# Optimization experiments

Hardware: AMD Instinct MI355X
Metric: run time of the kernel (lower is better)

Reference implementation:

```python
import jax, jax.numpy as jnp
import numpy as np

NUM_NODES = 50000
NUM_EDGES = 800000
DIM = 128


def setup_inputs() -> dict:
    key = jax.random.key(0)
    k0, k1, k2, k3 = jax.random.split(key, 4)
    edge_index = jax.random.randint(k0, (2, NUM_EDGES), 0, NUM_NODES, dtype=jnp.int64)
    emb = jax.random.normal(k1, (NUM_NODES, DIM), dtype=jnp.float32) * 0.02
    s = 1.0 / np.sqrt(DIM)
    W1 = jax.random.normal(k2, (DIM, DIM), dtype=jnp.float32) * s
    b1 = jnp.zeros((DIM,), dtype=jnp.float32)
    W2 = jax.random.normal(k3, (DIM, DIM), dtype=jnp.float32) * s
    b2 = jnp.zeros((DIM,), dtype=jnp.float32)
    return {"edge_index": edge_index, "emb": emb, "W1": W1, "b1": b1, "W2": W2, "b2": b2}


def gcn_conv(x, W, b, src, dst, num_nodes):
    # PyG GCNConv: h = x @ W; out = D^{-1/2}(A+I)D^{-1/2} h + b
    h = x @ W  # [N, D]
    deg = jnp.zeros((num_nodes,), h.dtype).at[dst].add(1.0) + 1.0  # +1 self-loop
    dis = jax.lax.rsqrt(deg)  # deg >= 1 always
    msg = h[src] * (dis[src] * dis[dst])[:, None]  # [E, D]
    agg = jax.ops.segment_sum(msg, dst, num_segments=num_nodes)
    agg = agg + h * (dis * dis)[:, None]  # self-loop term: norm = 1/deg
    return agg + b


def reference(edge_index, emb, W1, b1, W2, b2):
    src, dst = edge_index[0], edge_index[1]
    x = gcn_conv(emb, W1, b1, src, dst, NUM_NODES)
    x = jax.nn.relu(x)
    x = gcn_conv(x, W2, b2, src, dst, NUM_NODES)
    return x
```

## Files before the change

kernel.cpp:

```cpp
#include <hip/hip_runtime.h>
#include <hip/hip_fp16.h>

#define DIM 128
#define SEG 64
#define CAP 60

typedef _Float16 half8 __attribute__((ext_vector_type(8)));
typedef float floatx4 __attribute__((ext_vector_type(4)));


__global__ __launch_bounds__(256) void k_init_pack(unsigned short* __restrict__ csr, int N,
                                                   const float* __restrict__ W1,
                                                   const float* __restrict__ W2,
                                                   _Float16* __restrict__ Wp) {
    int i = blockIdx.x * 256 + threadIdx.x;
    int gs = gridDim.x * 256;
    if (i < 32768) {
        int sel = i >> 14;
        int flat = i & 16383;
        int f = flat >> 9;
        int rest = flat & 511;
        int lane = rest >> 3, j = rest & 7;
        int t = f >> 2, s = f & 3;
        int k = s * 32 + (lane >> 4) * 8 + j;
        int n = t * 16 + (lane & 15);
        const float* W = sel ? W2 : W1;
        Wp[(size_t)sel * 16384 + flat] = (_Float16)W[k * DIM + n];
    }
    const uint4 ff = make_uint4(~0u, ~0u, ~0u, ~0u);
    const uint4 head = make_uint4(0u, 0u, ~0u, ~0u);
    int total = N * 8;
    for (int j2 = i; j2 < total; j2 += gs)
        ((uint4*)csr)[j2] = ((j2 & 7) == 0) ? head : ff;
}


__global__ __launch_bounds__(256) void k_fill(const int* __restrict__ ei,
                                              unsigned short* __restrict__ csr,
                                              int E, int N) {
    int e = blockIdx.x * 256 + threadIdx.x;
    if (e < E) {
        int sv = ei[e];
        int dv = ei[E + e];
        if ((unsigned)sv < (unsigned)N && (unsigned)dv < (unsigned)N) {
            int pos = atomicAdd((int*)(csr + (size_t)dv * SEG), 1);
            if (pos < CAP) csr[(size_t)dv * SEG + 4 + pos] = (unsigned short)sv;
        }
    }
}


__global__ __launch_bounds__(256) void k_gemm1(const float* __restrict__ X,
                                               const unsigned short* __restrict__ csr,
                                               const _Float16* __restrict__ Wp,
                                               __half* __restrict__ out, int N) {
    __shared__ _Float16 ls[64 * 136];
    int tid = threadIdx.x;
    int w = tid >> 6, lane = tid & 63;
    int m = lane & 15, q = lane >> 4;
    int row0 = blockIdx.x * 64 + w * 16;

    int arow = row0 + m;
    bool okA = arow < N;
    half8 a[4];
#pragma unroll
    for (int s = 0; s < 4; ++s) {
        if (okA) {
            const float* Xa = X + (size_t)arow * DIM + s * 32 + q * 8;
            float4 f0 = *(const float4*)Xa;
            float4 f1 = *(const float4*)(Xa + 4);
            half8 h;
            h[0] = (_Float16)f0.x; h[1] = (_Float16)f0.y;
            h[2] = (_Float16)f0.z; h[3] = (_Float16)f0.w;
            h[4] = (_Float16)f1.x; h[5] = (_Float16)f1.y;
            h[6] = (_Float16)f1.z; h[7] = (_Float16)f1.w;
            a[s] = h;
        } else {
            a[s] = (half8)(_Float16)0.0f;
        }
    }
    int drow = row0 + q * 4;
    float dd[4];
#pragma unroll
    for (int r = 0; r < 4; ++r) {
        int rr2 = drow + r;
        int c = (rr2 < N) ? *(const int*)(csr + (size_t)rr2 * SEG) : 0;
        dd[r] = rsqrtf((float)c + 1.0f);
    }

    _Float16* lrow = ls + w * 16 * 136;
#pragma unroll
    for (int t = 0; t < 8; ++t) {
        floatx4 acc = {0.f, 0.f, 0.f, 0.f};
#pragma unroll
        for (int s = 0; s < 4; ++s) {
            half8 b = *(const half8*)(Wp + ((size_t)(t * 4 + s) * 64 + lane) * 8);
            acc = __builtin_amdgcn_mfma_f32_16x16x32_f16(a[s], b, acc, 0, 0, 0);
        }
#pragma unroll
        for (int r = 0; r < 4; ++r)
            lrow[(q * 4 + r) * 136 + t * 16 + m] = (_Float16)(acc[r] * dd[r]);
    }
    __syncthreads();

    int rr = lane >> 2, cc = (lane & 3) * 32;
    int grow = row0 + rr;
    if (grow < N) {
        const uint4* lsrc = (const uint4*)(lrow + rr * 136 + cc);
        uint4* gdst = (uint4*)((__half*)out + (size_t)grow * DIM + cc);
        gdst[0] = lsrc[0];
        gdst[1] = lsrc[1];
        gdst[2] = lsrc[2];
        gdst[3] = lsrc[3];
    }
}


__global__ __launch_bounds__(256) void k_aggemm(const __half* __restrict__ hn,
                                                const unsigned short* __restrict__ csr,
                                                const float* __restrict__ bias,
                                                const _Float16* __restrict__ Wp2,
                                                __half* __restrict__ hn2, int N) {
    __shared__ __align__(16) _Float16 As[16 * 136];
    __shared__ __align__(16) _Float16 Os[16 * 136];
    __shared__ float sdis[16];
    int tid = threadIdx.x;
    int slot = tid >> 4;
    int node = blockIdx.x * 16 + slot;
    int c8 = (tid & 15) << 3;

    float4 bv0 = *(const float4*)(bias + c8);
    float4 bv1 = *(const float4*)(bias + c8 + 4);
    float bb[8] = {bv0.x, bv0.y, bv0.z, bv0.w, bv1.x, bv1.y, bv1.z, bv1.w};
    const uint4 z4 = make_uint4(0u, 0u, 0u, 0u);
    const ushort4 sent = make_ushort4(0xFFFFu, 0xFFFFu, 0xFFFFu, 0xFFFFu);

    union { __half2 h[4]; uint4 u; } pu;
    pu.u = make_uint4(0u, 0u, 0u, 0u);
    float sc = 0.f;
    if (node < N) {
        const unsigned short* seg = csr + (size_t)node * SEG;
        int cnt = *(const int*)seg;
        uint4 selfv = *(const uint4*)(hn + (size_t)node * DIM + c8);
        sc = rsqrtf((float)cnt + 1.0f);
        int pcnt = (cnt + 3) & ~3;
        if (pcnt > CAP) pcnt = CAP;
        const unsigned short* slots = seg + 4;

        float acc[8];
#pragma unroll
        for (int j = 0; j < 8; ++j) acc[j] = 0.f;

        ushort4 ss = (pcnt > 0) ? *(const ushort4*)slots : sent;
        for (int e0 = 0; e0 < pcnt; e0 += 4) {
            ushort4 ssn = (e0 + 4 < pcnt) ? *(const ushort4*)(slots + e0 + 4) : sent;
            uint4 v0 = (ss.x != 0xFFFFu) ? *(const uint4*)(hn + (size_t)ss.x * DIM + c8) : z4;
            uint4 v1 = (ss.y != 0xFFFFu) ? *(const uint4*)(hn + (size_t)ss.y * DIM + c8) : z4;
            uint4 v2 = (ss.z != 0xFFFFu) ? *(const uint4*)(hn + (size_t)ss.z * DIM + c8) : z4;
            uint4 v3 = (ss.w != 0xFFFFu) ? *(const uint4*)(hn + (size_t)ss.w * DIM + c8) : z4;
            const __half2* h0 = (const __half2*)&v0;
            const __half2* h1 = (const __half2*)&v1;
            const __half2* h2 = (const __half2*)&v2;
            const __half2* h3 = (const __half2*)&v3;
#pragma unroll
            for (int j = 0; j < 4; ++j) {
                float2 f0 = __half22float2(h0[j]);
                float2 f1 = __half22float2(h1[j]);
                float2 f2 = __half22float2(h2[j]);
                float2 f3 = __half22float2(h3[j]);
                acc[2 * j]     += (f0.x + f1.x) + (f2.x + f3.x);
                acc[2 * j + 1] += (f0.y + f1.y) + (f2.y + f3.y);
            }
            ss = ssn;
        }

        const __half2* hs = (const __half2*)&selfv;
        float o[8];
#pragma unroll
        for (int j = 0; j < 4; ++j) {
            float2 fs = __half22float2(hs[j]);
            o[2 * j]     = (acc[2 * j]     + fs.x) * sc + bb[2 * j];
            o[2 * j + 1] = (acc[2 * j + 1] + fs.y) * sc + bb[2 * j + 1];
        }
        pu.h[0] = __floats2half2_rn(fmaxf(o[0], 0.f), fmaxf(o[1], 0.f));
        pu.h[1] = __floats2half2_rn(fmaxf(o[2], 0.f), fmaxf(o[3], 0.f));
        pu.h[2] = __floats2half2_rn(fmaxf(o[4], 0.f), fmaxf(o[5], 0.f));
        pu.h[3] = __floats2half2_rn(fmaxf(o[6], 0.f), fmaxf(o[7], 0.f));
    }
    *(uint4*)((char*)As + slot * 272 + (tid & 15) * 16) = pu.u;
    if ((tid & 15) == 0) sdis[slot] = sc;
    __syncthreads();

    int w = tid >> 6, lane = tid & 63;
    int m = lane & 15, q = lane >> 4;
    half8 a[4];
#pragma unroll
    for (int s = 0; s < 4; ++s)
        a[s] = *(const half8*)((const char*)As + m * 272 + s * 64 + q * 16);
    float dd[4];
#pragma unroll
    for (int r = 0; r < 4; ++r) dd[r] = sdis[q * 4 + r];

#pragma unroll
    for (int ti = 0; ti < 2; ++ti) {
        int t = w * 2 + ti;
        floatx4 acc2 = {0.f, 0.f, 0.f, 0.f};
#pragma unroll
        for (int s = 0; s < 4; ++s) {
            half8 b = *(const half8*)(Wp2 + ((size_t)(t * 4 + s) * 64 + lane) * 8);
            acc2 = __builtin_amdgcn_mfma_f32_16x16x32_f16(a[s], b, acc2, 0, 0, 0);
        }
#pragma unroll
        for (int r = 0; r < 4; ++r)
            Os[(q * 4 + r) * 136 + t * 16 + m] = (_Float16)(acc2[r] * dd[r]);
    }
    __syncthreads();

    int rr3 = tid >> 4, ci = tid & 15;
    int grow = blockIdx.x * 16 + rr3;
    if (grow < N)
        *(uint4*)((__half*)hn2 + (size_t)grow * DIM + ci * 8) =
            *(const uint4*)((const char*)Os + rr3 * 272 + ci * 16);
}


__global__ __launch_bounds__(256) void k_agg_out(const __half* __restrict__ hn,
                                                 const unsigned short* __restrict__ csr,
                                                 const float* __restrict__ bias,
                                                 float* __restrict__ outf, int N) {
    int tid = threadIdx.x;
    int node = (blockIdx.x * 256 + tid) >> 4;
    int c8 = (tid & 15) << 3;
    if (node >= N) return;

    float4 bv0 = *(const float4*)(bias + c8);
    float4 bv1 = *(const float4*)(bias + c8 + 4);
    float bb[8] = {bv0.x, bv0.y, bv0.z, bv0.w, bv1.x, bv1.y, bv1.z, bv1.w};
    const uint4 z4 = make_uint4(0u, 0u, 0u, 0u);
    const ushort4 sent = make_ushort4(0xFFFFu, 0xFFFFu, 0xFFFFu, 0xFFFFu);

    const unsigned short* seg = csr + (size_t)node * SEG;
    int cnt = *(const int*)seg;
    uint4 selfv = *(const uint4*)(hn + (size_t)node * DIM + c8);
    float sc = rsqrtf((float)cnt + 1.0f);
    int pcnt = (cnt + 3) & ~3;
    if (pcnt > CAP) pcnt = CAP;
    const unsigned short* slots = seg + 4;

    float acc[8];
#pragma unroll
    for (int j = 0; j < 8; ++j) acc[j] = 0.f;

    ushort4 ss = (pcnt > 0) ? *(const ushort4*)slots : sent;
    for (int e0 = 0; e0 < pcnt; e0 += 4) {
        ushort4 ssn = (e0 + 4 < pcnt) ? *(const ushort4*)(slots + e0 + 4) : sent;
        uint4 v0 = (ss.x != 0xFFFFu) ? *(const uint4*)(hn + (size_t)ss.x * DIM + c8) : z4;
        uint4 v1 = (ss.y != 0xFFFFu) ? *(const uint4*)(hn + (size_t)ss.y * DIM + c8) : z4;
        uint4 v2 = (ss.z != 0xFFFFu) ? *(const uint4*)(hn + (size_t)ss.z * DIM + c8) : z4;
        uint4 v3 = (ss.w != 0xFFFFu) ? *(const uint4*)(hn + (size_t)ss.w * DIM + c8) : z4;
        const __half2* h0 = (const __half2*)&v0;
        const __half2* h1 = (const __half2*)&v1;
        const __half2* h2 = (const __half2*)&v2;
        const __half2* h3 = (const __half2*)&v3;
#pragma unroll
        for (int j = 0; j < 4; ++j) {
            float2 f0 = __half22float2(h0[j]);
            float2 f1 = __half22float2(h1[j]);
            float2 f2 = __half22float2(h2[j]);
            float2 f3 = __half22float2(h3[j]);
            acc[2 * j]     += (f0.x + f1.x) + (f2.x + f3.x);
            acc[2 * j + 1] += (f0.y + f1.y) + (f2.y + f3.y);
        }
        ss = ssn;
    }

    const __half2* hs = (const __half2*)&selfv;
    float o[8];
#pragma unroll
    for (int j = 0; j < 4; ++j) {
        float2 fs = __half22float2(hs[j]);
        o[2 * j]     = (acc[2 * j]     + fs.x) * sc + bb[2 * j];
        o[2 * j + 1] = (acc[2 * j + 1] + fs.y) * sc + bb[2 * j + 1];
    }
    *(float4*)(outf + (size_t)node * DIM + c8) = make_float4(o[0], o[1], o[2], o[3]);
    *(float4*)(outf + (size_t)node * DIM + c8 + 4) = make_float4(o[4], o[5], o[6], o[7]);
}


extern "C" void kernel_launch(void* const* d_in, const int* in_sizes, int n_in,
                              void* d_out, int out_size, void* d_ws, size_t ws_size,
                              hipStream_t stream) {
    const int* ei = (const int*)d_in[0];
    const float* emb = (const float*)d_in[1];
    const float* W1 = (const float*)d_in[2];
    const float* b1 = (const float*)d_in[3];
    const float* W2 = (const float*)d_in[4];
    const float* b2 = (const float*)d_in[5];
    float* out = (float*)d_out;

    int E = in_sizes[0] / 2;
    int N = in_sizes[1] / DIM;

    char* p = (char*)d_ws;
    auto alloc = [&](size_t bytes) -> char* {
        char* r = p;
        p += (bytes + 255) & ~(size_t)255;
        return r;
    };
    unsigned short* csr = (unsigned short*)alloc((size_t)N * SEG * 2);
    __half* hn1         = (__half*)alloc((size_t)N * DIM * 2);
    __half* hn2         = (__half*)alloc((size_t)N * DIM * 2);
    _Float16* Wp        = (_Float16*)alloc(2 * 16384 * 2);

    const int GB = (N + 63) / 64;
    const int AB = (N + 15) / 16;

    k_init_pack<<<1024, 256, 0, stream>>>(csr, N, W1, W2, Wp);
    k_fill<<<(E + 255) / 256, 256, 0, stream>>>(ei, csr, E, N);
    k_gemm1<<<GB, 256, 0, stream>>>(emb, csr, Wp, hn1, N);
    k_aggemm<<<AB, 256, 0, stream>>>(hn1, csr, b1, Wp + 16384, hn2, N);
    k_agg_out<<<AB, 256, 0, stream>>>(hn2, csr, b2, out, N);
}
```

Before: 263.9 us.

## Fuse all GCN stages into one persistent cooperative kernel with grid syncs

Replaces the five separate kernel launches with a single cooperative persistent kernel. It runs CSR init, edge fill, first GEMM, fused aggregate+GEMM and final aggregation in sequence, separated by grid.sync barriers. This is meant to remove launch gaps and inter-kernel drain/fill overhead. In exchange the grid is capped at occupancy*CUs (up to 2048 blocks), so per-phase parallelism is limited and grid barriers add cost. The old multi-kernel path is kept as a fallback if the cooperative launch fails.

```diff
diff --git a/kernel.cpp b/kernel.cpp
--- a/kernel.cpp
+++ b/kernel.cpp
@@ -1,5 +1,8 @@
 #include <hip/hip_runtime.h>
 #include <hip/hip_fp16.h>
+#include <hip/hip_cooperative_groups.h>
+
+namespace cg = cooperative_groups;
 
 #define DIM 128
 #define SEG 64
@@ -9,17 +12,284 @@
 typedef float floatx4 __attribute__((ext_vector_type(4)));
 
 
-__global__ __launch_bounds__(256) void k_init_pack(unsigned short* __restrict__ csr, int N,
+__global__ __launch_bounds__(256, 4) void k_gcn(
+    const int* __restrict__ ei, const float* __restrict__ emb,
+    const float* __restrict__ W1, const float* __restrict__ b1,
+    const float* __restrict__ W2, const float* __restrict__ b2,
+    unsigned short* __restrict__ csr, __half* __restrict__ hn1,
+    __half* __restrict__ hn2, _Float16* __restrict__ Wp,
+    float* __restrict__ out, int E, int N)
+{
+    __shared__ __align__(16) char smem[64 * 136 * 2];
+    cg::grid_group grid = cg::this_grid();
+    const int tid = threadIdx.x;
+    const int nb = gridDim.x;
+    const int gtid = blockIdx.x * 256 + tid;
+    const int gs = nb * 256;
+
+    if (gtid < 32768) {
+        int sel = gtid >> 14, flat = gtid & 16383;
+        int f = flat >> 9, rest = flat & 511;
+        int lane = rest >> 3, j = rest & 7;
+        int t = f >> 2, s = f & 3;
+        int k = s * 32 + (lane >> 4) * 8 + j;
+        int n = t * 16 + (lane & 15);
+        const float* W = sel ? W2 : W1;
+        Wp[(size_t)sel * 16384 + flat] = (_Float16)W[k * DIM + n];
+    }
+    {
+        const uint4 ff = make_uint4(~0u, ~0u, ~0u, ~0u);
+        const uint4 head = make_uint4(0u, 0u, ~0u, ~0u);
+        int total = N * 8;
+        for (int j2 = gtid; j2 < total; j2 += gs)
+            ((uint4*)csr)[j2] = ((j2 & 7) == 0) ? head : ff;
+    }
+    __threadfence();
+    grid.sync();
+
+    for (int e = gtid; e < E; e += gs) {
+        int sv = ei[e];
+        int dv = ei[E + e];
+        if ((unsigned)sv < (unsigned)N && (unsigned)dv < (unsigned)N) {
+            int pos = atomicAdd((int*)(csr + (size_t)dv * SEG), 1);
+            if (pos < CAP) csr[(size_t)dv * SEG + 4 + pos] = (unsigned short)sv;
+        }
+    }
+    __threadfence();
+    grid.sync();
+
+    {
+        _Float16* ls = (_Float16*)smem;
+        int w = tid >> 6, lane = tid & 63;
+        int m = lane & 15, q = lane >> 4;
+        int nt = (N + 63) >> 6;
+        for (int tile = blockIdx.x; tile < nt; tile += nb) {
+            int row0 = tile * 64 + w * 16;
+            int arow = row0 + m;
+            bool okA = arow < N;
+            half8 a[4];
+#pragma unroll
+            for (int s = 0; s < 4; ++s) {
+                if (okA) {
+                    const float* Xa = emb + (size_t)arow * DIM + s * 32 + q * 8;
+                    float4 f0 = *(const float4*)Xa;
+                    float4 f1 = *(const float4*)(Xa + 4);
+                    half8 h;
+                    h[0] = (_Float16)f0.x; h[1] = (_Float16)f0.y;
+                    h[2] = (_Float16)f0.z; h[3] = (_Float16)f0.w;
+                    h[4] = (_Float16)f1.x; h[5] = (_Float16)f1.y;
+                    h[6] = (_Float16)f1.z; h[7] = (_Float16)f1.w;
+                    a[s] = h;
+                } else {
+                    a[s] = (half8)(_Float16)0.0f;
+                }
+            }
+            int drow = row0 + q * 4;
+            float dd[4];
+#pragma unroll
+            for (int r = 0; r < 4; ++r) {
+                int rr2 = drow + r;
+                int c = (rr2 < N) ? *(const int*)(csr + (size_t)rr2 * SEG) : 0;
+                dd[r] = rsqrtf((float)c + 1.0f);
+            }
+            _Float16* lrow = ls + w * 16 * 136;
+#pragma unroll
+            for (int t = 0; t < 8; ++t) {
+                floatx4 acc = {0.f, 0.f, 0.f, 0.f};
+#pragma unroll
+                for (int s = 0; s < 4; ++s) {
+                    half8 b = *(const half8*)(Wp + ((size_t)(t * 4 + s) * 64 + lane) * 8);
+                    acc = __builtin_amdgcn_mfma_f32_16x16x32_f16(a[s], b, acc, 0, 0, 0);
+                }
+#pragma unroll
+                for (int r = 0; r < 4; ++r)
+                    lrow[(q * 4 + r) * 136 + t * 16 + m] = (_Float16)(acc[r] * dd[r]);
+            }
+            __syncthreads();
+            int rr = lane >> 2, cc = (lane & 3) * 32;
+            int grow = row0 + rr;
+            if (grow < N) {
+                const uint4* lsrc = (const uint4*)(lrow + rr * 136 + cc);
+                uint4* gdst = (uint4*)((__half*)hn1 + (size_t)grow * DIM + cc);
+                gdst[0] = lsrc[0];
+                gdst[1] = lsrc[1];
+                gdst[2] = lsrc[2];
+                gdst[3] = lsrc[3];
+            }
+            __syncthreads();
+        }
+    }
+    __threadfence();
+    grid.sync();
+
+    {
+        _Float16* As = (_Float16*)smem;
+        _Float16* Os = (_Float16*)(smem + 4352);
+        float* sdis = (float*)(smem + 8704);
+        int slot = tid >> 4;
+        int c8 = (tid & 15) << 3;
+        int w = tid >> 6, lane = tid & 63;
+        int m = lane & 15, q = lane >> 4;
+        float4 bv0 = *(const float4*)(b1 + c8);
+        float4 bv1 = *(const float4*)(b1 + c8 + 4);
+        float bb[8] = {bv0.x, bv0.y, bv0.z, bv0.w, bv1.x, bv1.y, bv1.z, bv1.w};
+        const uint4 z4 = make_uint4(0u, 0u, 0u, 0u);
+        const ushort4 sent = make_ushort4(0xFFFFu, 0xFFFFu, 0xFFFFu, 0xFFFFu);
+        int nt = (N + 15) >> 4;
+        for (int tile = blockIdx.x; tile < nt; tile += nb) {
+            int node = tile * 16 + slot;
+            union { __half2 h[4]; uint4 u; } pu;
+            pu.u = make_uint4(0u, 0u, 0u, 0u);
+            float sc = 0.f;
+            if (node < N) {
+                const unsigned short* seg = csr + (size_t)node * SEG;
+                int cnt = *(const int*)seg;
+                uint4 selfv = *(const uint4*)(hn1 + (size_t)node * DIM + c8);
+                sc = rsqrtf((float)cnt + 1.0f);
+                int pcnt = (cnt + 3) & ~3;
+                if (pcnt > CAP) pcnt = CAP;
+                const unsigned short* slots = seg + 4;
+                float acc[8];
+#pragma unroll
+                for (int j = 0; j < 8; ++j) acc[j] = 0.f;
+                ushort4 ss = (pcnt > 0) ? *(const ushort4*)slots : sent;
+                for (int e0 = 0; e0 < pcnt; e0 += 4) {
+                    ushort4 ssn = (e0 + 4 < pcnt) ? *(const ushort4*)(slots + e0 + 4) : sent;
+                    uint4 v0 = (ss.x != 0xFFFFu) ? *(const uint4*)(hn1 + (size_t)ss.x * DIM + c8) : z4;
+                    uint4 v1 = (ss.y != 0xFFFFu) ? *(const uint4*)(hn1 + (size_t)ss.y * DIM + c8) : z4;
+                    uint4 v2 = (ss.z != 0xFFFFu) ? *(const uint4*)(hn1 + (size_t)ss.z * DIM + c8) : z4;
+                    uint4 v3 = (ss.w != 0xFFFFu) ? *(const uint4*)(hn1 + (size_t)ss.w * DIM + c8) : z4;
+                    const __half2* h0 = (const __half2*)&v0;
+                    const __half2* h1 = (const __half2*)&v1;
+                    const __half2* h2 = (const __half2*)&v2;
+                    const __half2* h3 = (const __half2*)&v3;
+#pragma unroll
+                    for (int j = 0; j < 4; ++j) {
+                        float2 f0 = __half22float2(h0[j]);
+                        float2 f1 = __half22float2(h1[j]);
+                        float2 f2 = __half22float2(h2[j]);
+                        float2 f3 = __half22float2(h3[j]);
+                        acc[2 * j]     += (f0.x + f1.x) + (f2.x + f3.x);
+                        acc[2 * j + 1] += (f0.y + f1.y) + (f2.y + f3.y);
+                    }
+                    ss = ssn;
+                }
+                const __half2* hs = (const __half2*)&selfv;
+                float o[8];
+#pragma unroll
+                for (int j = 0; j < 4; ++j) {
+                    float2 fs = __half22float2(hs[j]);
+                    o[2 * j]     = (acc[2 * j]     + fs.x) * sc + bb[2 * j];
+                    o[2 * j + 1] = (acc[2 * j + 1] + fs.y) * sc + bb[2 * j + 1];
+                }
+                pu.h[0] = __floats2half2_rn(fmaxf(o[0], 0.f), fmaxf(o[1], 0.f));
+                pu.h[1] = __floats2half2_rn(fmaxf(o[2], 0.f), fmaxf(o[3], 0.f));
+                pu.h[2] = __floats2half2_rn(fmaxf(o[4], 0.f), fmaxf(o[5], 0.f));
+                pu.h[3] = __floats2half2_rn(fmaxf(o[6], 0.f), fmaxf(o[7], 0.f));
+            }
+            *(uint4*)((char*)As + slot * 272 + (tid & 15) * 16) = pu.u;
+            if ((tid & 15) == 0) sdis[slot] = sc;
+            __syncthreads();
+
+            half8 a[4];
+#pragma unroll
+            for (int s = 0; s < 4; ++s)
+                a[s] = *(const half8*)((const char*)As + m * 272 + s * 64 + q * 16);
+            float dd[4];
+#pragma unroll
+            for (int r = 0; r < 4; ++r) dd[r] = sdis[q * 4 + r];
+#pragma unroll
+            for (int ti = 0; ti < 2; ++ti) {
+                int t = w * 2 + ti;
+                floatx4 acc2 = {0.f, 0.f, 0.f, 0.f};
+#pragma unroll
+                for (int s = 0; s < 4; ++s) {
+                    half8 b = *(const half8*)(Wp + 16384 + ((size_t)(t * 4 + s) * 64 + lane) * 8);
+                    acc2 = __builtin_amdgcn_mfma_f32_16x16x32_f16(a[s], b, acc2, 0, 0, 0);
+                }
+#pragma unroll
+                for (int r = 0; r < 4; ++r)
+                    Os[(q * 4 + r) * 136 + t * 16 + m] = (_Float16)(acc2[r] * dd[r]);
+            }
+            __syncthreads();
+
+            int rr3 = tid >> 4, ci = tid & 15;
+            int grow = tile * 16 + rr3;
+            if (grow < N)
+                *(uint4*)((__half*)hn2 + (size_t)grow * DIM + ci * 8) =
+                    *(const uint4*)((const char*)Os + rr3 * 272 + ci * 16);
+            __syncthreads();
+        }
+    }
+    __threadfence();
+    grid.sync();
+
+    {
+        int slot0 = gtid >> 4;
+        int c8 = (tid & 15) << 3;
+        int nslots = nb * 16;
+        float4 bv0 = *(const float4*)(b2 + c8);
+        float4 bv1 = *(const float4*)(b2 + c8 + 4);
+        float bb[8] = {bv0.x, bv0.y, bv0.z, bv0.w, bv1.x, bv1.y, bv1.z, bv1.w};
+        const uint4 z4 = make_uint4(0u, 0u, 0u, 0u);
+        const ushort4 sent = make_ushort4(0xFFFFu, 0xFFFFu, 0xFFFFu, 0xFFFFu);
+        for (int node = slot0; node < N; node += nslots) {
+            const unsigned short* seg = csr + (size_t)node * SEG;
+            int cnt = *(const int*)seg;
+            uint4 selfv = *(const uint4*)(hn2 + (size_t)node * DIM + c8);
+            float sc = rsqrtf((float)cnt + 1.0f);
+            int pcnt = (cnt + 3) & ~3;
+            if (pcnt > CAP) pcnt = CAP;
+            const unsigned short* slots = seg + 4;
+            float acc[8];
+#pragma unroll
+            for (int j = 0; j < 8; ++j) acc[j] = 0.f;
+            ushort4 ss = (pcnt > 0) ? *(const ushort4*)slots : sent;
+            for (int e0 = 0; e0 < pcnt; e0 += 4) {
+                ushort4 ssn = (e0 + 4 < pcnt) ? *(const ushort4*)(slots + e0 + 4) : sent;
+                uint4 v0 = (ss.x != 0xFFFFu) ? *(const uint4*)(hn2 + (size_t)ss.x * DIM + c8) : z4;
+                uint4 v1 = (ss.y != 0xFFFFu) ? *(const uint4*)(hn2 + (size_t)ss.y * DIM + c8) : z4;
+                uint4 v2 = (ss.z != 0xFFFFu) ? *(const uint4*)(hn2 + (size_t)ss.z * DIM + c8) : z4;
+                uint4 v3 = (ss.w != 0xFFFFu) ? *(const uint4*)(hn2 + (size_t)ss.w * DIM + c8) : z4;
+                const __half2* h0 = (const __half2*)&v0;
+                const __half2* h1 = (const __half2*)&v1;
+                const __half2* h2 = (const __half2*)&v2;
+                const __half2* h3 = (const __half2*)&v3;
+#pragma unroll
+                for (int j = 0; j < 4; ++j) {
+                    float2 f0 = __half22float2(h0[j]);
+                    float2 f1 = __half22float2(h1[j]);
+                    float2 f2 = __half22float2(h2[j]);
+                    float2 f3 = __half22float2(h3[j]);
+                    acc[2 * j]     += (f0.x + f1.x) + (f2.x + f3.x);
+                    acc[2 * j + 1] += (f0.y + f1.y) + (f2.y + f3.y);
+                }
+                ss = ssn;
+            }
+            const __half2* hs = (const __half2*)&selfv;
+            float o[8];
+#pragma unroll
+            for (int j = 0; j < 4; ++j) {
+                float2 fs = __half22float2(hs[j]);
+                o[2 * j]     = (acc[2 * j]     + fs.x) * sc + bb[2 * j];
+                o[2 * j + 1] = (acc[2 * j + 1] + fs.y) * sc + bb[2 * j + 1];
+            }
+            *(float4*)(out + (size_t)node * DIM + c8) = make_float4(o[0], o[1], o[2], o[3]);
+            *(float4*)(out + (size_t)node * DIM + c8 + 4) = make_float4(o[4], o[5], o[6], o[7]);
+        }
+    }
+}
+
+
+__global__ __launch_bounds__(256) void f_init_pack(unsigned short* __restrict__ csr, int N,
                                                    const float* __restrict__ W1,
                                                    const float* __restrict__ W2,
                                                    _Float16* __restrict__ Wp) {
     int i = blockIdx.x * 256 + threadIdx.x;
     int gs = gridDim.x * 256;
     if (i < 32768) {
-        int sel = i >> 14;
-        int flat = i & 16383;
-        int f = flat >> 9;
-        int rest = flat & 511;
+        int sel = i >> 14, flat = i & 16383;
+        int f = flat >> 9, rest = flat & 511;
         int lane = rest >> 3, j = rest & 7;
         int t = f >> 2, s = f & 3;
         int k = s * 32 + (lane >> 4) * 8 + j;
@@ -34,8 +304,7 @@
         ((uint4*)csr)[j2] = ((j2 & 7) == 0) ? head : ff;
 }
 
-
-__global__ __launch_bounds__(256) void k_fill(const int* __restrict__ ei,
+__global__ __launch_bounds__(256) void f_fill(const int* __restrict__ ei,
                                               unsigned short* __restrict__ csr,
                                               int E, int N) {
     int e = blockIdx.x * 256 + threadIdx.x;
@@ -49,8 +318,7 @@
     }
 }
 
-
-__global__ __launch_bounds__(256) void k_gemm1(const float* __restrict__ X,
+__global__ __launch_bounds__(256) void f_gemm1(const float* __restrict__ X,
                                                const unsigned short* __restrict__ csr,
                                                const _Float16* __restrict__ Wp,
                                                __half* __restrict__ out, int N) {
@@ -115,8 +383,7 @@
     }
 }
 
-
-__global__ __launch_bounds__(256) void k_aggemm(const __half* __restrict__ hn,
+__global__ __launch_bounds__(256) void f_aggemm(const __half* __restrict__ hn,
                                                 const unsigned short* __restrict__ csr,
                                                 const float* __restrict__ bias,
                                                 const _Float16* __restrict__ Wp2,
@@ -223,8 +490,7 @@
             *(const uint4*)((const char*)Os + rr3 * 272 + ci * 16);
 }
 
-
-__global__ __launch_bounds__(256) void k_agg_out(const __half* __restrict__ hn,
+__global__ __launch_bounds__(256) void f_agg_out(const __half* __restrict__ hn,
                                                  const unsigned short* __restrict__ csr,
                                                  const float* __restrict__ bias,
                                                  float* __restrict__ outf, int N) {
@@ -312,12 +578,39 @@
     __half* hn2         = (__half*)alloc((size_t)N * DIM * 2);
     _Float16* Wp        = (_Float16*)alloc(2 * 16384 * 2);
 
-    const int GB = (N + 63) / 64;
-    const int AB = (N + 15) / 16;
-
-    k_init_pack<<<1024, 256, 0, stream>>>(csr, N, W1, W2, Wp);
-    k_fill<<<(E + 255) / 256, 256, 0, stream>>>(ei, csr, E, N);
-    k_gemm1<<<GB, 256, 0, stream>>>(emb, csr, Wp, hn1, N);
-    k_aggemm<<<AB, 256, 0, stream>>>(hn1, csr, b1, Wp + 16384, hn2, N);
-    k_agg_out<<<AB, 256, 0, stream>>>(hn2, csr, b2, out, N);
+    static int coop_grid = -2;
+    if (coop_grid == -2) {
+        int dev = 0, ncu = 0, occ = 0;
+        if (hipGetDevice(&dev) == hipSuccess &&
+            hipDeviceGetAttribute(&ncu, hipDeviceAttributeMultiprocessorCount, dev) == hipSuccess &&
+            hipOccupancyMaxActiveBlocksPerMultiprocessor(&occ, k_gcn, 256, 0) == hipSuccess &&
+            occ >= 1 && ncu >= 1) {
+            long g = (long)occ * (long)ncu;
+            coop_grid = (int)(g > 2048 ? 2048 : g);
+        } else {
+            coop_grid = -1;
+        }
+    }
+
+    bool done = false;
+    if (coop_grid > 0) {
+        void* args[] = {&ei, &emb, &W1, &b1, &W2, &b2, &csr, &hn1, &hn2, &Wp, &out, &E, &N};
+        hipError_t err = hipLaunchCooperativeKernel((const void*)k_gcn, dim3(coop_grid),
+                                                    dim3(256), args, 0, stream);
+        if (err == hipSuccess) {
+            done = true;
+        } else {
+            coop_grid = -1;
+        }
+    }
+
+    if (!done) {
+        const int GB = (N + 63) / 64;
+        const int AB = (N + 15) / 16;
+        f_init_pack<<<1024, 256, 0, stream>>>(csr, N, W1, W2, Wp);
+        f_fill<<<(E + 255) / 256, 256, 0, stream>>>(ei, csr, E, N);
+        f_gemm1<<<GB, 256, 0, stream>>>(emb, csr, Wp, hn1, N);
+        f_aggemm<<<AB, 256, 0, stream>>>(hn1, csr, b1, Wp + 16384, hn2, N);
+        f_agg_out<<<AB, 256, 0, stream>>>(hn2, csr, b2, out, N);
+    }
 }
```

Result: slower. 704.8 us (+167.1%).
